# Optimization experiments

Measured on AMD Instinct MI355X. Metric: run time of the kernel, lower is better.

Reference implementation:

```python
import jax, jax.numpy as jnp
import numpy as np

N_NODES = 100000
N_EDGES = 1200000
D = 64


def setup_inputs() -> dict:
    key = jax.random.key(0)
    ks = jax.random.split(key, 11)
    feats = jax.random.normal(ks[0], (N_NODES, D), dtype=jnp.float32)
    src = jax.random.randint(ks[1], (N_EDGES,), 0, N_NODES)
    dst = jax.random.randint(ks[2], (N_EDGES,), 0, N_NODES)
    s = 0.1  # small init scale
    W1 = jax.random.normal(ks[3], (D, D), dtype=jnp.float32) * s
    b1 = jnp.zeros((D,), dtype=jnp.float32)
    Wr1 = jax.random.normal(ks[4], (D, D), dtype=jnp.float32) * s
    br1 = jnp.zeros((D,), dtype=jnp.float32)
    W2 = jax.random.normal(ks[5], (D, D), dtype=jnp.float32) * s
    b2 = jnp.zeros((D,), dtype=jnp.float32)
    Wr2 = jax.random.normal(ks[6], (D, D), dtype=jnp.float32) * s
    br2 = jnp.zeros((D,), dtype=jnp.float32)
    return {"feats": feats, "W1": W1, "b1": b1, "Wr1": Wr1, "br1": br1,
            "W2": W2, "b2": b2, "Wr2": Wr2, "br2": br2,
            "src": src, "dst": dst}


def _gcn_layer(x, W, b, Wr, br, src, dst):
    # dgl GraphConv(norm='none'): aggregate sum of transformed neighbor feats + bias, then ReLU
    xw = x @ W                                        # [N, D]
    agg = jax.ops.segment_sum(xw[src], dst, num_segments=x.shape[0])  # gather-scatter
    conv = jax.nn.relu(agg + b)
    # residual branch: activation(Linear(feats))
    res = jax.nn.relu(x @ Wr + br)
    return conv + res  # dropout=0.0, batchnorm=False


def reference(feats, W1, b1, Wr1, br1, W2, b2, Wr2, br2, src, dst):
    h = _gcn_layer(feats, W1, b1, Wr1, br1, src, dst)
    h = _gcn_layer(h, W2, b2, Wr2, br2, src, dst)
    return h
```

## Files before the change

kernel.cpp:

```cpp
#include <hip/hip_runtime.h>

#define D 64
#define NBMAX 256
#define BCHUNK 4096
#define CAP 8192
#define CAP_PACK 12288

typedef unsigned short ushort_t;
typedef __attribute__((ext_vector_type(8))) short bf16x8;
typedef __attribute__((ext_vector_type(4))) float floatx4;

static __device__ __forceinline__ ushort_t f2bf(float x) {
  unsigned u = __float_as_uint(x);
  unsigned r = (u + 0x7FFF + ((u >> 16) & 1)) >> 16;
  return (ushort_t)r;
}
static __device__ __forceinline__ float bf2f(ushort_t u) {
  return __uint_as_float(((unsigned)u) << 16);
}

static __device__ __forceinline__ void addrow(const uint4 v, float2& a0,
                                              float2& a1, float2& a2,
                                              float2& a3) {
  a0.x += __uint_as_float(v.x << 16);
  a0.y += __uint_as_float(v.x & 0xffff0000u);
  a1.x += __uint_as_float(v.y << 16);
  a1.y += __uint_as_float(v.y & 0xffff0000u);
  a2.x += __uint_as_float(v.z << 16);
  a2.y += __uint_as_float(v.z & 0xffff0000u);
  a3.x += __uint_as_float(v.w << 16);
  a3.y += __uint_as_float(v.w & 0xffff0000u);
}

#define GLOAD4(T0, T1, T2, T3, IR, OFF, CB)                                    \
  do {                                                                         \
    const int s0_ = __shfl((IR), gbase + (OFF) + 0, 64);                       \
    const int s1_ = __shfl((IR), gbase + (OFF) + 1, 64);                       \
    const int s2_ = __shfl((IR), gbase + (OFF) + 2, 64);                       \
    const int s3_ = __shfl((IR), gbase + (OFF) + 3, 64);                       \
    T0 = ((CB) + 0 < m) ? *(const uint4*)(tab + ((size_t)s0_ << 6) + off16)    \
                        : z4;                                                  \
    T1 = ((CB) + 1 < m) ? *(const uint4*)(tab + ((size_t)s1_ << 6) + off16)    \
                        : z4;                                                  \
    T2 = ((CB) + 2 < m) ? *(const uint4*)(tab + ((size_t)s2_ << 6) + off16)    \
                        : z4;                                                  \
    T3 = ((CB) + 3 < m) ? *(const uint4*)(tab + ((size_t)s3_ << 6) + off16)    \
                        : z4;                                                  \
  } while (0)

#define ACC4(T0, T1, T2, T3)    \
  do {                          \
    addrow(T0, c0, c1, c2, c3); \
    addrow(T1, c0, c1, c2, c3); \
    addrow(T2, c0, c1, c2, c3); \
    addrow(T3, c0, c1, c2, c3); \
  } while (0)

static __device__ __forceinline__ void gather_node8(
    const ushort_t* __restrict__ tab, const int* __restrict__ csr_src, int e0,
    int e1, int sub8, int gbase, float2& c0, float2& c1, float2& c2,
    float2& c3) {
  const int off16 = sub8 << 3;
  const int m = e1 - e0;
  const int ir0 = (e0 + 0 + sub8 < e1) ? csr_src[e0 + 0 + sub8] : 0;
  const int ir1 = (e0 + 8 + sub8 < e1) ? csr_src[e0 + 8 + sub8] : 0;
  const int ir2 = (e0 + 16 + sub8 < e1) ? csr_src[e0 + 16 + sub8] : 0;
  const int ir3 = (e0 + 24 + sub8 < e1) ? csr_src[e0 + 24 + sub8] : 0;
  int mm = m;
  mm = max(mm, __shfl_xor(mm, 8, 64));
  mm = max(mm, __shfl_xor(mm, 16, 64));
  mm = max(mm, __shfl_xor(mm, 32, 64));
  const int nch = __builtin_amdgcn_readfirstlane(min((mm + 3) >> 2, 8));
  const uint4 z4 = make_uint4(0, 0, 0, 0);
  uint4 A0, A1, A2, A3, B0, B1, B2, B3;
  if (nch > 0) {
    GLOAD4(A0, A1, A2, A3, ir0, 0, 0);
    if (nch > 1) GLOAD4(B0, B1, B2, B3, ir0, 4, 4);
    ACC4(A0, A1, A2, A3);
    if (nch > 1) {
      if (nch > 2) GLOAD4(A0, A1, A2, A3, ir1, 0, 8);
      ACC4(B0, B1, B2, B3);
      if (nch > 2) {
        if (nch > 3) GLOAD4(B0, B1, B2, B3, ir1, 4, 12);
        ACC4(A0, A1, A2, A3);
        if (nch > 3) {
          if (nch > 4) GLOAD4(A0, A1, A2, A3, ir2, 0, 16);
          ACC4(B0, B1, B2, B3);
          if (nch > 4) {
            if (nch > 5) GLOAD4(B0, B1, B2, B3, ir2, 4, 20);
            ACC4(A0, A1, A2, A3);
            if (nch > 5) {
              if (nch > 6) GLOAD4(A0, A1, A2, A3, ir3, 0, 24);
              ACC4(B0, B1, B2, B3);
              if (nch > 6) {
                if (nch > 7) GLOAD4(B0, B1, B2, B3, ir3, 4, 28);
                ACC4(A0, A1, A2, A3);
                if (nch > 7) ACC4(B0, B1, B2, B3);
              }
            }
          }
        }
      }
    }
  }
  for (int eb = e0 + 32; eb < e1; ++eb) {
    const int ii = csr_src[eb];
    const uint4 tv = *(const uint4*)(tab + ((size_t)ii << 6) + off16);
    addrow(tv, c0, c1, c2, c3);
  }
}

__global__ __launch_bounds__(256) void gemm_res_mfma_kernel(
    const float* __restrict__ x, const float* __restrict__ W,
    const float* __restrict__ Wr, const float* __restrict__ br,
    ushort_t* __restrict__ xw, ushort_t* __restrict__ res, int n_nodes,
    int* __restrict__ gtail, int* __restrict__ off_tail, int n_edges) {
  if (blockIdx.x == 0) {
    if (threadIdx.x < NBMAX) gtail[threadIdx.x] = (int)threadIdx.x * CAP_PACK;
    if (threadIdx.x == 0) *off_tail = n_edges;
  }
  const int lane = threadIdx.x & 63;
  const int wid = threadIdx.x >> 6;
  const int sub = lane & 15;
  const int q = lane >> 4;

  bf16x8 bW[4][2], bR[4][2];
#pragma unroll
  for (int t = 0; t < 4; ++t) {
#pragma unroll
    for (int s = 0; s < 2; ++s) {
      bf16x8 fw, fr;
#pragma unroll
      for (int j = 0; j < 8; ++j) {
        const int k = s * 32 + q * 8 + j;
        const int c = t * 16 + sub;
        fw[j] = (short)f2bf(W[k * D + c]);
        fr[j] = (short)f2bf(Wr[k * D + c]);
      }
      bW[t][s] = fw;
      bR[t][s] = fr;
    }
  }
  float brv[4];
#pragma unroll
  for (int t = 0; t < 4; ++t) brv[t] = br[t * 16 + sub];

  const int n_tiles = (n_nodes + 15) >> 4;
  const int wave_id = blockIdx.x * 4 + wid;
  const int n_waves = gridDim.x * 4;
  for (int tile = wave_id; tile < n_tiles; tile += n_waves) {
    const int n0 = tile << 4;
    const bool full = (n0 + 16 <= n_nodes);
    bf16x8 a0h, a0l, a1h, a1l;
    float v[16];
    if (full) {
      const float* xp = x + (size_t)(n0 + sub) * D + q * 8;
      *(float4*)(v + 0)  = *(const float4*)(xp);
      *(float4*)(v + 4)  = *(const float4*)(xp + 4);
      *(float4*)(v + 8)  = *(const float4*)(xp + 32);
      *(float4*)(v + 12) = *(const float4*)(xp + 36);
    } else {
      const bool ok = (n0 + sub) < n_nodes;
      const float* xp = x + (size_t)(n0 + sub) * D + q * 8;
#pragma unroll
      for (int j = 0; j < 8; ++j) {
        v[j] = ok ? xp[j] : 0.f;
        v[8 + j] = ok ? xp[32 + j] : 0.f;
      }
    }
#pragma unroll
    for (int j = 0; j < 8; ++j) {
      const ushort_t h0 = f2bf(v[j]);
      a0h[j] = (short)h0;
      a0l[j] = (short)f2bf(v[j] - bf2f(h0));
      const ushort_t h1 = f2bf(v[8 + j]);
      a1h[j] = (short)h1;
      a1l[j] = (short)f2bf(v[8 + j] - bf2f(h1));
    }
    floatx4 accW[4], accR[4];
#pragma unroll
    for (int t = 0; t < 4; ++t) {
      accW[t] = (floatx4){0.f, 0.f, 0.f, 0.f};
      accR[t] = (floatx4){0.f, 0.f, 0.f, 0.f};
    }
#pragma unroll
    for (int t = 0; t < 4; ++t) {
      accW[t] = __builtin_amdgcn_mfma_f32_16x16x32_bf16(a0h, bW[t][0], accW[t], 0, 0, 0);
      accW[t] = __builtin_amdgcn_mfma_f32_16x16x32_bf16(a0l, bW[t][0], accW[t], 0, 0, 0);
      accW[t] = __builtin_amdgcn_mfma_f32_16x16x32_bf16(a1h, bW[t][1], accW[t], 0, 0, 0);
      accW[t] = __builtin_amdgcn_mfma_f32_16x16x32_bf16(a1l, bW[t][1], accW[t], 0, 0, 0);
      accR[t] = __builtin_amdgcn_mfma_f32_16x16x32_bf16(a0h, bR[t][0], accR[t], 0, 0, 0);
      accR[t] = __builtin_amdgcn_mfma_f32_16x16x32_bf16(a0l, bR[t][0], accR[t], 0, 0, 0);
      accR[t] = __builtin_amdgcn_mfma_f32_16x16x32_bf16(a1h, bR[t][1], accR[t], 0, 0, 0);
      accR[t] = __builtin_amdgcn_mfma_f32_16x16x32_bf16(a1l, bR[t][1], accR[t], 0, 0, 0);
    }
    if (full) {
#pragma unroll
      for (int t = 0; t < 4; ++t) {
#pragma unroll
        for (int i = 0; i < 4; ++i) {
          const size_t r = (size_t)(n0 + q * 4 + i) * D + t * 16 + sub;
          xw[r] = f2bf(accW[t][i]);
          res[r] = f2bf(fmaxf(accR[t][i] + brv[t], 0.f));
        }
      }
    } else {
#pragma unroll
      for (int t = 0; t < 4; ++t) {
#pragma unroll
        for (int i = 0; i < 4; ++i) {
          const int rr = n0 + q * 4 + i;
          if (rr < n_nodes) {
            const size_t r = (size_t)rr * D + t * 16 + sub;
            xw[r] = f2bf(accW[t][i]);
            res[r] = f2bf(fmaxf(accR[t][i] + brv[t], 0.f));
          }
        }
      }
    }
  }
}

__global__ __launch_bounds__(256) void binpack_kernel(
    const int* __restrict__ src, const int* __restrict__ dst,
    int* __restrict__ gtail, unsigned* __restrict__ packed, int n_edges) {
  __shared__ int start[NBMAX], cur[NBMAX], gpos[NBMAX];
  __shared__ unsigned sorted[BCHUNK];
  __shared__ unsigned char bktid[BCHUNK];
  const int t = threadIdx.x;
  const int nchunk = (n_edges + BCHUNK - 1) / BCHUNK;
  for (int c = blockIdx.x; c < nchunk; c += gridDim.x) {
    cur[t] = 0;
    __syncthreads();
    const int e0 = c * BCHUNK;
    const int m = min(BCHUNK, n_edges - e0);
    int bk[16];
    unsigned pk[16];
#pragma unroll
    for (int k = 0; k < 16; ++k) {
      const int e = e0 + k * 256 + t;
      if (e < n_edges) {
        const int d = dst[e];
        const int s = src[e];
        bk[k] = d >> 9;
        pk[k] = ((unsigned)(d & 511) << 23) | (unsigned)s;
        atomicAdd(&cur[bk[k]], 1);
      } else {
        bk[k] = -1;
      }
    }
    __syncthreads();
    const int h = cur[t];
    start[t] = h;
    __syncthreads();
    for (int off = 1; off < NBMAX; off <<= 1) {
      const int v = (t >= off) ? start[t - off] : 0;
      __syncthreads();
      start[t] += v;
      __syncthreads();
    }
    const int excl = start[t] - h;
    __syncthreads();
    start[t] = excl;
    cur[t] = excl;
    __syncthreads();
#pragma unroll
    for (int k = 0; k < 16; ++k) {
      if (bk[k] >= 0) {
        const int pos = atomicAdd(&cur[bk[k]], 1);
        sorted[pos] = pk[k];
        bktid[pos] = (unsigned char)bk[k];
      }
    }
    __syncthreads();
    if (h > 0) gpos[t] = atomicAdd(&gtail[t], h);
    __syncthreads();
    for (int j = t; j < m; j += 256) {
      const int b = bktid[j];
      packed[gpos[b] + j - start[b]] = sorted[j];
    }
    __syncthreads();
  }
}

__global__ __launch_bounds__(256) void bucket_csr_kernel(
    const unsigned* __restrict__ packed, const int* __restrict__ gtail,
    int* __restrict__ csr_off, int* __restrict__ csr_src, int n_nodes,
    int nbuckets) {
  __shared__ int scnt[NBMAX], sexc[NBMAX];
  __shared__ int sc[2][512];
  __shared__ int cur[512];
  __shared__ unsigned outbuf[CAP];
  const int b = blockIdx.x;
  const int t = threadIdx.x;
  const int cb = (t < nbuckets) ? (gtail[t] - t * CAP_PACK) : 0;
  scnt[t] = cb;
  sexc[t] = cb;
  __syncthreads();
  for (int off = 1; off < NBMAX; off <<= 1) {
    const int v = (t >= off) ? sexc[t - off] : 0;
    __syncthreads();
    sexc[t] += v;
    __syncthreads();
  }
  sexc[t] -= scnt[t];
  __syncthreads();
  const int base = sexc[b];
  const int cntE = scnt[b];
  const unsigned* pk = packed + (size_t)b * CAP_PACK;

  const int n0 = b << 9;
  const int nn = min(512, n_nodes - n0);
  cur[t] = 0;
  cur[t + 256] = 0;
  __syncthreads();
  for (int i = t; i < cntE; i += 256) atomicAdd(&cur[pk[i] >> 23], 1);
  __syncthreads();
  const int h0 = cur[t];
  const int h1 = cur[t + 256];
  sc[0][t] = h0;
  sc[0][t + 256] = h1;
  __syncthreads();
  int pin = 0;
  for (int off = 1; off < 512; off <<= 1) {
    sc[1 - pin][t] = sc[pin][t] + ((t >= off) ? sc[pin][t - off] : 0);
    sc[1 - pin][t + 256] =
        sc[pin][t + 256] + ((t + 256 >= off) ? sc[pin][t + 256 - off] : 0);
    __syncthreads();
    pin ^= 1;
  }
  const int excl0 = sc[pin][t] - h0;
  const int excl1 = sc[pin][t + 256] - h1;
  if (t < nn) csr_off[n0 + t] = base + excl0;
  if (t + 256 < nn) csr_off[n0 + t + 256] = base + excl1;
  cur[t] = excl0;
  cur[t + 256] = excl1;
  __syncthreads();
  if (cntE <= CAP) {
    for (int i = t; i < cntE; i += 256) {
      const unsigned u = pk[i];
      const int pos = atomicAdd(&cur[u >> 23], 1);
      outbuf[pos] = u & 0x7FFFFFu;
    }
    __syncthreads();
    for (int j = t; j < cntE; j += 256) csr_src[base + j] = (int)outbuf[j];
  } else {
    for (int i = t; i < cntE; i += 256) {
      const unsigned u = pk[i];
      const int pos = atomicAdd(&cur[u >> 23], 1);
      csr_src[base + pos] = (int)(u & 0x7FFFFFu);
    }
  }
}

__global__ __launch_bounds__(256, 6) void gather_gemm_kernel(
    const ushort_t* __restrict__ xw1, const ushort_t* __restrict__ res1,
    const float* __restrict__ b1v, const int* __restrict__ csr_off,
    const int* __restrict__ csr_src, const float* __restrict__ W2,
    const float* __restrict__ Wr2, const float* __restrict__ br2,
    ushort_t* __restrict__ xw2, ushort_t* __restrict__ res2, int n_nodes) {
  const int lane = threadIdx.x & 63;
  const int w = threadIdx.x >> 6;
  const int sub = lane & 15;
  const int q = lane >> 4;
  const int sub8 = lane & 7;
  const int g = lane >> 3;
  const int gbase = lane & 56;
  __shared__ float h_tile[32][68];
  __shared__ bf16x8 wfrag[2][8][64];
  __shared__ float b1s[64];

#pragma unroll
  for (int s = 0; s < 2; ++s) {
    bf16x8 fw, fr;
#pragma unroll
    for (int j = 0; j < 8; ++j) {
      const int k = s * 32 + q * 8 + j;
      const int c = w * 16 + sub;
      fw[j] = (short)f2bf(W2[k * D + c]);
      fr[j] = (short)f2bf(Wr2[k * D + c]);
    }
    wfrag[0][w * 2 + s][lane] = fw;
    wfrag[1][w * 2 + s][lane] = fr;
  }
  if (threadIdx.x < 64) b1s[threadIdx.x] = b1v[threadIdx.x];
  const float brl2 = br2[w * 16 + sub];
  __syncthreads();

  const int n_tiles = (n_nodes + 31) >> 5;
  for (int tile = blockIdx.x; tile < n_tiles; tile += gridDim.x) {
    const int n0 = tile << 5;
    const int nb = n0 + w * 8;
    const int offv = csr_off[min(nb + (lane < 9 ? lane : 8), n_nodes)];
    const int e0 = __shfl(offv, g, 64);
    const int e1 = __shfl(offv, g + 1, 64);
    float2 c0 = {0.f, 0.f}, c1 = {0.f, 0.f}, c2 = {0.f, 0.f}, c3 = {0.f, 0.f};
    gather_node8(xw1, csr_src, e0, e1, sub8, gbase, c0, c1, c2, c3);
    const int n = nb + g;
    const int row = (w << 3) + g;
    if (n < n_nodes) {
      const uint4 rv = *(const uint4*)(res1 + ((size_t)n << 6) + (sub8 << 3));
      const float2 bz0 = *(const float2*)(&b1s[sub8 * 8 + 0]);
      const float2 bz1 = *(const float2*)(&b1s[sub8 * 8 + 2]);
      const float2 bz2 = *(const float2*)(&b1s[sub8 * 8 + 4]);
      const float2 bz3 = *(const float2*)(&b1s[sub8 * 8 + 6]);
      float4 lo, hi;
      lo.x = fmaxf(c0.x + bz0.x, 0.f) + __uint_as_float(rv.x << 16);
      lo.y = fmaxf(c0.y + bz0.y, 0.f) + __uint_as_float(rv.x & 0xffff0000u);
      lo.z = fmaxf(c1.x + bz1.x, 0.f) + __uint_as_float(rv.y << 16);
      lo.w = fmaxf(c1.y + bz1.y, 0.f) + __uint_as_float(rv.y & 0xffff0000u);
      hi.x = fmaxf(c2.x + bz2.x, 0.f) + __uint_as_float(rv.z << 16);
      hi.y = fmaxf(c2.y + bz2.y, 0.f) + __uint_as_float(rv.z & 0xffff0000u);
      hi.z = fmaxf(c3.x + bz3.x, 0.f) + __uint_as_float(rv.w << 16);
      hi.w = fmaxf(c3.y + bz3.y, 0.f) + __uint_as_float(rv.w & 0xffff0000u);
      *(float4*)(&h_tile[row][sub8 * 8]) = lo;
      *(float4*)(&h_tile[row][sub8 * 8 + 4]) = hi;
    } else {
      *(float4*)(&h_tile[row][sub8 * 8]) = make_float4(0.f, 0.f, 0.f, 0.f);
      *(float4*)(&h_tile[row][sub8 * 8 + 4]) = make_float4(0.f, 0.f, 0.f, 0.f);
    }
    __syncthreads();
#pragma unroll
    for (int st = 0; st < 2; ++st) {
      const float* hrow = &h_tile[st * 16 + sub][0];
      bf16x8 a0h, a0l, a1h, a1l;
      {
        const float4 p0 = *(const float4*)(hrow + q * 8);
        const float4 p1 = *(const float4*)(hrow + q * 8 + 4);
        const float vv[8] = {p0.x, p0.y, p0.z, p0.w, p1.x, p1.y, p1.z, p1.w};
#pragma unroll
        for (int j = 0; j < 8; ++j) {
          const ushort_t h0 = f2bf(vv[j]);
          a0h[j] = (short)h0;
          a0l[j] = (short)f2bf(vv[j] - bf2f(h0));
        }
      }
      {
        const float4 p2 = *(const float4*)(hrow + 32 + q * 8);
        const float4 p3 = *(const float4*)(hrow + 32 + q * 8 + 4);
        const float vv[8] = {p2.x, p2.y, p2.z, p2.w, p3.x, p3.y, p3.z, p3.w};
#pragma unroll
        for (int j = 0; j < 8; ++j) {
          const ushort_t h1 = f2bf(vv[j]);
          a1h[j] = (short)h1;
          a1l[j] = (short)f2bf(vv[j] - bf2f(h1));
        }
      }
      const bf16x8 w0 = wfrag[0][w * 2 + 0][lane];
      const bf16x8 w1 = wfrag[0][w * 2 + 1][lane];
      const bf16x8 r0 = wfrag[1][w * 2 + 0][lane];
      const bf16x8 r1 = wfrag[1][w * 2 + 1][lane];
      floatx4 accW = (floatx4){0.f, 0.f, 0.f, 0.f};
      floatx4 accR = (floatx4){0.f, 0.f, 0.f, 0.f};
      accW = __builtin_amdgcn_mfma_f32_16x16x32_bf16(a0h, w0, accW, 0, 0, 0);
      accW = __builtin_amdgcn_mfma_f32_16x16x32_bf16(a0l, w0, accW, 0, 0, 0);
      accW = __builtin_amdgcn_mfma_f32_16x16x32_bf16(a1h, w1, accW, 0, 0, 0);
      accW = __builtin_amdgcn_mfma_f32_16x16x32_bf16(a1l, w1, accW, 0, 0, 0);
      accR = __builtin_amdgcn_mfma_f32_16x16x32_bf16(a0h, r0, accR, 0, 0, 0);
      accR = __builtin_amdgcn_mfma_f32_16x16x32_bf16(a0l, r0, accR, 0, 0, 0);
      accR = __builtin_amdgcn_mfma_f32_16x16x32_bf16(a1h, r1, accR, 0, 0, 0);
      accR = __builtin_amdgcn_mfma_f32_16x16x32_bf16(a1l, r1, accR, 0, 0, 0);
#pragma unroll
      for (int i = 0; i < 4; ++i) {
        const int rr = n0 + st * 16 + q * 4 + i;
        if (rr < n_nodes) {
          const size_t r = (size_t)rr * D + w * 16 + sub;
          xw2[r] = f2bf(accW[i]);
          res2[r] = f2bf(fmaxf(accR[i] + brl2, 0.f));
        }
      }
    }
    __syncthreads();
  }
}

__global__ __launch_bounds__(256) void gather_combine_kernel(
    const ushort_t* __restrict__ xw, const ushort_t* __restrict__ res,
    const float* __restrict__ b, const int* __restrict__ csr_off,
    const int* __restrict__ csr_src, float* __restrict__ out, int n_nodes) {
  const int lane = threadIdx.x & 63;
  const int w = threadIdx.x >> 6;
  const int sub8 = lane & 7;
  const int g = lane >> 3;
  const int gbase = lane & 56;
  const int n_tiles = (n_nodes + 31) >> 5;
  for (int tile = blockIdx.x; tile < n_tiles; tile += gridDim.x) {
    const int nb = (tile << 5) + w * 8;
    const int offv = csr_off[min(nb + (lane < 9 ? lane : 8), n_nodes)];
    const int e0 = __shfl(offv, g, 64);
    const int e1 = __shfl(offv, g + 1, 64);
    float2 c0 = {0.f, 0.f}, c1 = {0.f, 0.f}, c2 = {0.f, 0.f}, c3 = {0.f, 0.f};
    gather_node8(xw, csr_src, e0, e1, sub8, gbase, c0, c1, c2, c3);
    const int n = nb + g;
    if (n < n_nodes) {
      const uint4 rv = *(const uint4*)(res + ((size_t)n << 6) + (sub8 << 3));
      const float4 blo = *(const float4*)(b + sub8 * 8);
      const float4 bhi = *(const float4*)(b + sub8 * 8 + 4);
      float4 lo, hi;
      lo.x = fmaxf(c0.x + blo.x, 0.f) + __uint_as_float(rv.x << 16);
      lo.y = fmaxf(c0.y + blo.y, 0.f) + __uint_as_float(rv.x & 0xffff0000u);
      lo.z = fmaxf(c1.x + blo.z, 0.f) + __uint_as_float(rv.y << 16);
      lo.w = fmaxf(c1.y + blo.w, 0.f) + __uint_as_float(rv.y & 0xffff0000u);
      hi.x = fmaxf(c2.x + bhi.x, 0.f) + __uint_as_float(rv.z << 16);
      hi.y = fmaxf(c2.y + bhi.y, 0.f) + __uint_as_float(rv.z & 0xffff0000u);
      hi.z = fmaxf(c3.x + bhi.z, 0.f) + __uint_as_float(rv.w << 16);
      hi.w = fmaxf(c3.y + bhi.w, 0.f) + __uint_as_float(rv.w & 0xffff0000u);
      *(float4*)(out + ((size_t)n << 6) + sub8 * 8) = lo;
      *(float4*)(out + ((size_t)n << 6) + sub8 * 8 + 4) = hi;
    }
  }
}

extern "C" void kernel_launch(void* const* d_in, const int* in_sizes, int n_in,
                              void* d_out, int out_size, void* d_ws, size_t ws_size,
                              hipStream_t stream) {
  const float* feats = (const float*)d_in[0];
  const float* W1  = (const float*)d_in[1];
  const float* b1  = (const float*)d_in[2];
  const float* Wr1 = (const float*)d_in[3];
  const float* br1 = (const float*)d_in[4];
  const float* W2  = (const float*)d_in[5];
  const float* b2  = (const float*)d_in[6];
  const float* Wr2 = (const float*)d_in[7];
  const float* br2 = (const float*)d_in[8];
  const int* src = (const int*)d_in[9];
  const int* dst = (const int*)d_in[10];
  const int n_nodes = in_sizes[0] / D;
  const int n_edges = in_sizes[9];
  float* out = (float*)d_out;

  const int nbuckets = (n_nodes + 511) >> 9;

  ushort_t* xw1 = (ushort_t*)d_ws;
  ushort_t* res1 = xw1 + (size_t)n_nodes * D;
  ushort_t* xw2 = res1 + (size_t)n_nodes * D;
  ushort_t* res2 = xw2 + (size_t)n_nodes * D;
  int* csr_off = (int*)(res2 + (size_t)n_nodes * D);
  int* csr_src = csr_off + (n_nodes + 1);
  int* gtail = csr_src + n_edges;
  unsigned* packed = (unsigned*)(gtail + NBMAX);

  const int tiles32 = (n_nodes + 31) / 32;
  const int gblocks = tiles32 < 16384 ? tiles32 : 16384;
  const int nchunk = (n_edges + BCHUNK - 1) / BCHUNK;
  const int pblocks = nchunk < 1024 ? nchunk : 1024;
  dim3 blk(256);

  gemm_res_mfma_kernel<<<1024, blk, 0, stream>>>(
      feats, W1, Wr1, br1, xw1, res1, n_nodes, gtail, csr_off + n_nodes, n_edges);
  binpack_kernel<<<pblocks, blk, 0, stream>>>(src, dst, gtail, packed, n_edges);
  bucket_csr_kernel<<<nbuckets, blk, 0, stream>>>(packed, gtail, csr_off,
                                                  csr_src, n_nodes, nbuckets);
  gather_gemm_kernel<<<gblocks, blk, 0, stream>>>(
      xw1, res1, b1, csr_off, csr_src, W2, Wr2, br2, xw2, res2, n_nodes);
  gather_combine_kernel<<<gblocks, blk, 0, stream>>>(
      xw2, res2, b2, csr_off, csr_src, out, n_nodes);
}
```

Measured before the change: 254.5 us.

## Merge edge bin-packing and first-layer GEMM into one concurrent prep kernel

Combines the independent binpack and first-layer GEMM/residual kernels into one launch. The first pblocks blocks bucket the edges and the remaining blocks do the MFMA GEMM, so the two phases can overlap on the GPU instead of running back to back. The gtail initialisation moves to a hipMemsetAsync, bucket offsets are now relative to zero, and the csr_off tail write moves into bucket_csr. The launch-bounds occupancy hint on gather_gemm is also dropped. The merged kernel now reserves the binpack shared memory for the GEMM blocks too, which may lower their occupancy.

Result: faster. 228.1 us (-10.4%).

```diff
diff --git a/kernel.cpp b/kernel.cpp
--- a/kernel.cpp
+++ b/kernel.cpp
@@ -110,14 +110,72 @@
   }
 }
 
-__global__ __launch_bounds__(256) void gemm_res_mfma_kernel(
+__global__ __launch_bounds__(256) void prep_kernel(
     const float* __restrict__ x, const float* __restrict__ W,
     const float* __restrict__ Wr, const float* __restrict__ br,
     ushort_t* __restrict__ xw, ushort_t* __restrict__ res, int n_nodes,
-    int* __restrict__ gtail, int* __restrict__ off_tail, int n_edges) {
-  if (blockIdx.x == 0) {
-    if (threadIdx.x < NBMAX) gtail[threadIdx.x] = (int)threadIdx.x * CAP_PACK;
-    if (threadIdx.x == 0) *off_tail = n_edges;
+    const int* __restrict__ src, const int* __restrict__ dst,
+    int* __restrict__ gtail, unsigned* __restrict__ packed, int n_edges,
+    int pblocks) {
+  __shared__ int start[NBMAX], cur[NBMAX], gpos[NBMAX];
+  __shared__ unsigned sorted[BCHUNK];
+  __shared__ unsigned char bktid[BCHUNK];
+  if ((int)blockIdx.x < pblocks) {
+    const int t = threadIdx.x;
+    const int nchunk = (n_edges + BCHUNK - 1) / BCHUNK;
+    for (int c = blockIdx.x; c < nchunk; c += pblocks) {
+      cur[t] = 0;
+      __syncthreads();
+      const int e0 = c * BCHUNK;
+      const int m = min(BCHUNK, n_edges - e0);
+      int bk[16];
+      unsigned pk[16];
+#pragma unroll
+      for (int k = 0; k < 16; ++k) {
+        const int e = e0 + k * 256 + t;
+        if (e < n_edges) {
+          const int d = dst[e];
+          const int s = src[e];
+          bk[k] = d >> 9;
+          pk[k] = ((unsigned)(d & 511) << 23) | (unsigned)s;
+          atomicAdd(&cur[bk[k]], 1);
+        } else {
+          bk[k] = -1;
+        }
+      }
+      __syncthreads();
+      const int h = cur[t];
+      start[t] = h;
+      __syncthreads();
+      for (int off = 1; off < NBMAX; off <<= 1) {
+        const int v = (t >= off) ? start[t - off] : 0;
+        __syncthreads();
+        start[t] += v;
+        __syncthreads();
+      }
+      const int excl = start[t] - h;
+      __syncthreads();
+      start[t] = excl;
+      cur[t] = excl;
+      __syncthreads();
+#pragma unroll
+      for (int k = 0; k < 16; ++k) {
+        if (bk[k] >= 0) {
+          const int pos = atomicAdd(&cur[bk[k]], 1);
+          sorted[pos] = pk[k];
+          bktid[pos] = (unsigned char)bk[k];
+        }
+      }
+      __syncthreads();
+      if (h > 0) gpos[t] = t * CAP_PACK + atomicAdd(&gtail[t], h);
+      __syncthreads();
+      for (int j = t; j < m; j += 256) {
+        const int b = bktid[j];
+        packed[gpos[b] + j - start[b]] = sorted[j];
+      }
+      __syncthreads();
+    }
+    return;
   }
   const int lane = threadIdx.x & 63;
   const int wid = threadIdx.x >> 6;
@@ -145,9 +203,10 @@
 #pragma unroll
   for (int t = 0; t < 4; ++t) brv[t] = br[t * 16 + sub];
 
+  const int gb = (int)gridDim.x - pblocks;
   const int n_tiles = (n_nodes + 15) >> 4;
-  const int wave_id = blockIdx.x * 4 + wid;
-  const int n_waves = gridDim.x * 4;
+  const int wave_id = ((int)blockIdx.x - pblocks) * 4 + wid;
+  const int n_waves = gb * 4;
   for (int tile = wave_id; tile < n_tiles; tile += n_waves) {
     const int n0 = tile << 4;
     const bool full = (n0 + 16 <= n_nodes);
@@ -221,79 +280,18 @@
   }
 }
 
-__global__ __launch_bounds__(256) void binpack_kernel(
-    const int* __restrict__ src, const int* __restrict__ dst,
-    int* __restrict__ gtail, unsigned* __restrict__ packed, int n_edges) {
-  __shared__ int start[NBMAX], cur[NBMAX], gpos[NBMAX];
-  __shared__ unsigned sorted[BCHUNK];
-  __shared__ unsigned char bktid[BCHUNK];
-  const int t = threadIdx.x;
-  const int nchunk = (n_edges + BCHUNK - 1) / BCHUNK;
-  for (int c = blockIdx.x; c < nchunk; c += gridDim.x) {
-    cur[t] = 0;
-    __syncthreads();
-    const int e0 = c * BCHUNK;
-    const int m = min(BCHUNK, n_edges - e0);
-    int bk[16];
-    unsigned pk[16];
-#pragma unroll
-    for (int k = 0; k < 16; ++k) {
-      const int e = e0 + k * 256 + t;
-      if (e < n_edges) {
-        const int d = dst[e];
-        const int s = src[e];
-        bk[k] = d >> 9;
-        pk[k] = ((unsigned)(d & 511) << 23) | (unsigned)s;
-        atomicAdd(&cur[bk[k]], 1);
-      } else {
-        bk[k] = -1;
-      }
-    }
-    __syncthreads();
-    const int h = cur[t];
-    start[t] = h;
-    __syncthreads();
-    for (int off = 1; off < NBMAX; off <<= 1) {
-      const int v = (t >= off) ? start[t - off] : 0;
-      __syncthreads();
-      start[t] += v;
-      __syncthreads();
-    }
-    const int excl = start[t] - h;
-    __syncthreads();
-    start[t] = excl;
-    cur[t] = excl;
-    __syncthreads();
-#pragma unroll
-    for (int k = 0; k < 16; ++k) {
-      if (bk[k] >= 0) {
-        const int pos = atomicAdd(&cur[bk[k]], 1);
-        sorted[pos] = pk[k];
-        bktid[pos] = (unsigned char)bk[k];
-      }
-    }
-    __syncthreads();
-    if (h > 0) gpos[t] = atomicAdd(&gtail[t], h);
-    __syncthreads();
-    for (int j = t; j < m; j += 256) {
-      const int b = bktid[j];
-      packed[gpos[b] + j - start[b]] = sorted[j];
-    }
-    __syncthreads();
-  }
-}
-
 __global__ __launch_bounds__(256) void bucket_csr_kernel(
     const unsigned* __restrict__ packed, const int* __restrict__ gtail,
     int* __restrict__ csr_off, int* __restrict__ csr_src, int n_nodes,
-    int nbuckets) {
+    int nbuckets, int n_edges) {
   __shared__ int scnt[NBMAX], sexc[NBMAX];
   __shared__ int sc[2][512];
   __shared__ int cur[512];
   __shared__ unsigned outbuf[CAP];
   const int b = blockIdx.x;
   const int t = threadIdx.x;
-  const int cb = (t < nbuckets) ? (gtail[t] - t * CAP_PACK) : 0;
+  if (b == 0 && t == 0) csr_off[n_nodes] = n_edges;
+  const int cb = (t < nbuckets) ? gtail[t] : 0;
   scnt[t] = cb;
   sexc[t] = cb;
   __syncthreads();
@@ -353,7 +351,7 @@
   }
 }
 
-__global__ __launch_bounds__(256, 6) void gather_gemm_kernel(
+__global__ __launch_bounds__(256) void gather_gemm_kernel(
     const ushort_t* __restrict__ xw1, const ushort_t* __restrict__ res1,
     const float* __restrict__ b1v, const int* __restrict__ csr_off,
     const int* __restrict__ csr_src, const float* __restrict__ W2,
@@ -546,11 +544,13 @@
   const int pblocks = nchunk < 1024 ? nchunk : 1024;
   dim3 blk(256);
 
-  gemm_res_mfma_kernel<<<1024, blk, 0, stream>>>(
-      feats, W1, Wr1, br1, xw1, res1, n_nodes, gtail, csr_off + n_nodes, n_edges);
-  binpack_kernel<<<pblocks, blk, 0, stream>>>(src, dst, gtail, packed, n_edges);
+  hipMemsetAsync(gtail, 0, NBMAX * sizeof(int), stream);
+  prep_kernel<<<pblocks + 1024, blk, 0, stream>>>(
+      feats, W1, Wr1, br1, xw1, res1, n_nodes, src, dst, gtail, packed,
+      n_edges, pblocks);
   bucket_csr_kernel<<<nbuckets, blk, 0, stream>>>(packed, gtail, csr_off,
-                                                  csr_src, n_nodes, nbuckets);
+                                                  csr_src, n_nodes, nbuckets,
+                                                  n_edges);
   gather_gemm_kernel<<<gblocks, blk, 0, stream>>>(
       xw1, res1, b1, csr_off, csr_src, W2, Wr2, br2, xw2, res2, n_nodes);
   gather_combine_kernel<<<gblocks, blk, 0, stream>>>(
```
